# Performance work log

Measured on AMD Instinct MI355X. Metric: run time of the kernel, lower is better.

The kernel has to match this reference:

```python
import jax, jax.numpy as jnp
import numpy as np

B, P, E, D, A = 128, 196, 2048, 512, 512


def setup_inputs() -> dict:
    key = jax.random.key(0)
    ks = jax.random.split(key, 8)
    s = lambda fan_in: 1.0 / np.sqrt(fan_in)
    return {
        "encoder_out": jax.random.normal(ks[0], (B, P, E), jnp.float32),
        "decoder_hidden": jax.random.normal(ks[1], (B, D), jnp.float32),
        "We": jax.random.uniform(ks[2], (E, A), jnp.float32, -s(E), s(E)),
        "be": jax.random.uniform(ks[3], (A,), jnp.float32, -s(E), s(E)),
        "Wd": jax.random.uniform(ks[4], (D, A), jnp.float32, -s(D), s(D)),
        "bd": jax.random.uniform(ks[5], (A,), jnp.float32, -s(D), s(D)),
        "Wf": jax.random.uniform(ks[6], (A, 1), jnp.float32, -s(A), s(A)),
        "bf": jax.random.uniform(ks[7], (1,), jnp.float32, -s(A), s(A)),
    }


def reference(encoder_out, decoder_hidden, We, be, Wd, bd, Wf, bf):
    # att1: [B, P, A]
    att1 = jnp.einsum("bpe,ea->bpa", encoder_out, We) + be
    # att2: [B, A]
    att2 = decoder_hidden @ Wd + bd
    # additive attention scores: [B, P]
    att = (jax.nn.relu(att1 + att2[:, None, :]) @ Wf + bf)[..., 0]
    alpha = jax.nn.softmax(att, axis=1)  # softmax over pixels
    # weighted sum over pixels: [B, E]
    awe = jnp.einsum("bpe,bp->be", encoder_out, alpha)
    return awe, alpha
```

## Files before the change

### kernel.cpp

```cpp
#include <hip/hip_runtime.h>
#include <hip/hip_bf16.h>

typedef __attribute__((ext_vector_type(2))) unsigned int u32x2;
typedef __attribute__((ext_vector_type(4))) float f32x4;
typedef __attribute__((ext_vector_type(4))) unsigned int u32x4;
typedef __attribute__((ext_vector_type(8))) short s16x8;

#define B_  128
#define P_  196
#define E_  2048
#define D_  512
#define A_  512
#define M_  (B_*P_)
#define MT  112

typedef __attribute__((address_space(1))) const unsigned int gu32;
typedef __attribute__((address_space(3))) unsigned int lu32;
__device__ __forceinline__ void gl_lds16(const void* g, void* l) {
  __builtin_amdgcn_global_load_lds((gu32*)g, (lu32*)l, 16, 0, 0);
}

#define WAIT_VM3() asm volatile("s_waitcnt vmcnt(3)" ::: "memory")
#define WAIT_VM0() asm volatile("s_waitcnt vmcnt(0)" ::: "memory")
#define WAIT_LGKM0() asm volatile("s_waitcnt lgkmcnt(0)" ::: "memory")

__global__ void we_conv_kernel(const float* __restrict__ We,
                               unsigned short* __restrict__ WeTs) {
  __shared__ float tile[32][33];
  const int tx = threadIdx.x, ty = threadIdx.y;
  const int a0 = blockIdx.x * 32, e0 = blockIdx.y * 32;
  tile[ty][tx] = We[(e0 + ty) * A_ + a0 + tx];
  __syncthreads();
  const float v = tile[tx][ty];
  const unsigned int u = __float_as_uint(v);
  const unsigned short r = (unsigned short)((u + 0x7fffu + ((u >> 16) & 1u)) >> 16);
  const int a = a0 + ty;
  const int kt = blockIdx.y;
  const int c8 = tx >> 3, j = tx & 7;
  const int dest = ((a * 32 + c8 * 8) ^ ((a & 7) << 3)) + j;
  WeTs[kt * 16384 + dest] = r;
}

__global__ void att2_kernel(const float* __restrict__ h, const float* __restrict__ Wd,
                            const float* __restrict__ bd, const float* __restrict__ be,
                            float* __restrict__ att2pb) {
  const int b = blockIdx.x;
  const int t = threadIdx.x;
  __shared__ float hs[D_];
  hs[t] = h[b * D_ + t];
  hs[t + 256] = h[b * D_ + t + 256];
  __syncthreads();
  float a0 = 0.f, a1 = 0.f;
  for (int d = 0; d < D_; ++d) {
    const float hv = hs[d];
    a0 = fmaf(hv, Wd[d * A_ + t], a0);
    a1 = fmaf(hv, Wd[d * A_ + t + 256], a1);
  }
  att2pb[b * A_ + t] = a0 + bd[t] + be[t];
  att2pb[b * A_ + t + 256] = a1 + bd[t + 256] + be[t + 256];
}

__device__ inline unsigned pk2(float a, float b) {
  union { __hip_bfloat162 h; unsigned u; } cv;
  cv.h = __float22bfloat162_rn(make_float2(a, b));
  return cv.u;
}
__device__ __forceinline__ s16x8 ldsr(const unsigned short* p) {
  return *(const s16x8*)p;
}
#define MF(a, b, c) c = __builtin_amdgcn_mfma_f32_16x16x32_bf16(a, b, c, 0, 0, 0)

__launch_bounds__(1024, 4)
__global__ void score_kernel(const float* __restrict__ enc,
                             const unsigned short* __restrict__ WeTs,
                             const float* __restrict__ att2pb,
                             const float* __restrict__ Wf,
                             float* __restrict__ att_part) {
  __shared__ unsigned short Bh[3][512 * 32];
  __shared__ unsigned short Ahs[3][128 * 32];

  const int bid = blockIdx.x;
  const int m0 = bid * MT;

  const int t = threadIdx.x;
  const int lane = t & 63, w = t >> 6;
  const int wn = w * 32;

  const int ar = t >> 3, ac4 = t & 7;
  const int arc = ar < MT ? ar : MT - 1;
  const float* aptr = enc + (size_t)(m0 + arc) * E_ + ac4 * 4;
  const int awz = (ar * 32 + ac4 * 4) ^ ((ar & 7) << 3);

  const int doff = t * 8;

  const int q = lane >> 4, fr = lane & 15;
  const int fx = (fr & 7) << 3;
  int fa[7], fb[2];
#pragma unroll
  for (int i = 0; i < 7; ++i) fa[i] = ((i * 16 + fr) * 32 + q * 8) ^ fx;
#pragma unroll
  for (int j = 0; j < 2; ++j) fb[j] = ((wn + j * 16 + fr) * 32 + q * 8) ^ fx;

  const f32x4 zero = {0.f, 0.f, 0.f, 0.f};
  f32x4 acc[7][2];
#pragma unroll
  for (int mi = 0; mi < 7; ++mi) {
    acc[mi][0] = zero;
    acc[mi][1] = zero;
  }

  unsigned short *bAc = &Ahs[0][0], *bA1 = &Ahs[1][0], *bA2 = &Ahs[2][0];
  unsigned short *bBc = &Bh[0][0],  *bB1 = &Bh[1][0],  *bB2 = &Bh[2][0];

  f32x4 aC, aN;

  {
    aC = *(const f32x4*)(aptr);
    gl_lds16(WeTs + doff, bBc + doff);
    gl_lds16(WeTs + 8192 + doff, bBc + 8192 + doff);
    aN = *(const f32x4*)(aptr + 32);
    gl_lds16(WeTs + 16384 + doff, bB1 + doff);
    gl_lds16(WeTs + 16384 + 8192 + doff, bB1 + 8192 + doff);
    u32x2 av; av[0] = pk2(aC[0], aC[1]); av[1] = pk2(aC[2], aC[3]);
    *(u32x2*)(bAc + awz) = av;
    aC = aN;
    WAIT_VM3();
    WAIT_LGKM0();
    __builtin_amdgcn_s_barrier();
  }

  for (int it = 0; it < 62; ++it) {
    const int kof = (it + 2) * 32;
    aN = *(const f32x4*)(aptr + kof);
    const unsigned short* sb = WeTs + (size_t)(it + 2) * 16384;
    gl_lds16(sb + doff, bB2 + doff);
    gl_lds16(sb + 8192 + doff, bB2 + 8192 + doff);

    {
      s16x8 fbh0 = ldsr(bBc + fb[0]);
      s16x8 fbh1 = ldsr(bBc + fb[1]);
      __builtin_amdgcn_s_setprio(1);
#pragma unroll
      for (int mi = 0; mi < 7; ++mi) {
        const s16x8 fah = ldsr(bAc + fa[mi]);
        MF(fah, fbh0, acc[mi][0]);
        MF(fah, fbh1, acc[mi][1]);
      }
      __builtin_amdgcn_s_setprio(0);
    }

    {
      u32x2 av; av[0] = pk2(aC[0], aC[1]); av[1] = pk2(aC[2], aC[3]);
      *(u32x2*)(bA1 + awz) = av;
    }
    aC = aN;

    WAIT_VM3();
    WAIT_LGKM0();
    __builtin_amdgcn_s_barrier();

    unsigned short* tmp;
    tmp = bAc; bAc = bA1; bA1 = bA2; bA2 = tmp;
    tmp = bBc; bBc = bB1; bB1 = bB2; bB2 = tmp;
  }

  {
    s16x8 fbh0 = ldsr(bBc + fb[0]);
    s16x8 fbh1 = ldsr(bBc + fb[1]);
#pragma unroll
    for (int mi = 0; mi < 7; ++mi) {
      const s16x8 fah = ldsr(bAc + fa[mi]);
      MF(fah, fbh0, acc[mi][0]);
      MF(fah, fbh1, acc[mi][1]);
    }
    u32x2 av; av[0] = pk2(aC[0], aC[1]); av[1] = pk2(aC[2], aC[3]);
    *(u32x2*)(bA1 + awz) = av;
    WAIT_VM0();
    WAIT_LGKM0();
    __builtin_amdgcn_s_barrier();
  }

  {
    s16x8 fbh0 = ldsr(bB1 + fb[0]);
    s16x8 fbh1 = ldsr(bB1 + fb[1]);
#pragma unroll
    for (int mi = 0; mi < 7; ++mi) {
      const s16x8 fah = ldsr(bA1 + fa[mi]);
      MF(fah, fbh0, acc[mi][0]);
      MF(fah, fbh1, acc[mi][1]);
    }
  }

  const int colL = wn + fr;
  const float wf0 = Wf[colL], wf1 = Wf[colL + 16];
#pragma unroll
  for (int mi = 0; mi < 7; ++mi) {
    const int rowb = m0 + mi * 16 + (q << 2);
#pragma unroll
    for (int r = 0; r < 4; ++r) {
      const int row = rowb + r;
      const int bb = row / P_;
      const float* a2 = att2pb + bb * A_ + colL;
      float s = fmaxf(acc[mi][0][r] + a2[0], 0.f) * wf0
              + fmaxf(acc[mi][1][r] + a2[16], 0.f) * wf1;
#pragma unroll
      for (int off = 1; off < 16; off <<= 1) s += __shfl_xor(s, off);
      if (fr == 0) att_part[row * 16 + w] = s;
    }
  }
}

__global__ void softmax_awe_kernel(const float* __restrict__ enc,
                                   const float* __restrict__ att_part,
                                   float* __restrict__ out) {
  const int bid = blockIdx.x;
  const int b = bid >> 1, ch = bid & 1;
  const int t = threadIdx.x;
  __shared__ float sm[256];
  __shared__ float alpha_s[P_];

  float av = -1e30f;
  if (t < P_) {
    const float* apt = att_part + (b * P_ + t) * 16;
    float s = 0.f;
#pragma unroll
    for (int i = 0; i < 16; ++i) s += apt[i];
    av = s;
  }
  sm[t] = av;
  __syncthreads();
  for (int st = 128; st > 0; st >>= 1) {
    if (t < st) sm[t] = fmaxf(sm[t], sm[t + st]);
    __syncthreads();
  }
  const float mx = sm[0];
  __syncthreads();
  float ev = 0.f;
  if (t < P_) ev = __expf(av - mx);
  sm[t] = ev;
  __syncthreads();
  for (int st = 128; st > 0; st >>= 1) {
    if (t < st) sm[t] += sm[t + st];
    __syncthreads();
  }
  const float denom = sm[0];
  const float al = ev / denom;
  if (t < P_) {
    alpha_s[t] = al;
    if (ch == 0) out[B_ * E_ + b * P_ + t] = al;
  }
  __syncthreads();

  const int e0 = ch * 1024 + t * 4;
  const float* ebase = enc + (size_t)b * P_ * E_ + e0;
  f32x4 acc = {0.f, 0.f, 0.f, 0.f};
  for (int p = 0; p < P_; ++p) {
    const f32x4 v = *(const f32x4*)(ebase + (size_t)p * E_);
    const float a = alpha_s[p];
    acc.x += a * v.x; acc.y += a * v.y; acc.z += a * v.z; acc.w += a * v.w;
  }
  *(f32x4*)(out + b * E_ + e0) = acc;
}

extern "C" void kernel_launch(void* const* d_in, const int* in_sizes, int n_in,
                              void* d_out, int out_size, void* d_ws, size_t ws_size,
                              hipStream_t stream) {
  const float* enc = (const float*)d_in[0];
  const float* h   = (const float*)d_in[1];
  const float* We  = (const float*)d_in[2];
  const float* be  = (const float*)d_in[3];
  const float* Wd  = (const float*)d_in[4];
  const float* bd  = (const float*)d_in[5];
  const float* Wf  = (const float*)d_in[6];
  float* out = (float*)d_out;

  float* att2pb = (float*)d_ws;
  float* att_part = att2pb + B_ * A_;
  unsigned short* WeTs = (unsigned short*)(att_part + M_ * 16);

  we_conv_kernel<<<dim3(A_ / 32, E_ / 32), dim3(32, 32), 0, stream>>>(We, WeTs);
  att2_kernel<<<B_, 256, 0, stream>>>(h, Wd, bd, be, att2pb);
  score_kernel<<<M_ / MT, 1024, 0, stream>>>(enc, WeTs, att2pb, Wf, att_part);
  softmax_awe_kernel<<<B_ * 2, 256, 0, stream>>>(enc, att_part, out);
}
```

Before: 130.2 us.

## Load We fragments directly into registers instead of staging through LDS

```diff
diff --git a/kernel.cpp b/kernel.cpp
--- a/kernel.cpp
+++ b/kernel.cpp
@@ -3,7 +3,6 @@
 
 typedef __attribute__((ext_vector_type(2))) unsigned int u32x2;
 typedef __attribute__((ext_vector_type(4))) float f32x4;
-typedef __attribute__((ext_vector_type(4))) unsigned int u32x4;
 typedef __attribute__((ext_vector_type(8))) short s16x8;
 
 #define B_  128
@@ -14,18 +13,10 @@
 #define M_  (B_*P_)
 #define MT  112
 
-typedef __attribute__((address_space(1))) const unsigned int gu32;
-typedef __attribute__((address_space(3))) unsigned int lu32;
-__device__ __forceinline__ void gl_lds16(const void* g, void* l) {
-  __builtin_amdgcn_global_load_lds((gu32*)g, (lu32*)l, 16, 0, 0);
-}
-
-#define WAIT_VM3() asm volatile("s_waitcnt vmcnt(3)" ::: "memory")
-#define WAIT_VM0() asm volatile("s_waitcnt vmcnt(0)" ::: "memory")
 #define WAIT_LGKM0() asm volatile("s_waitcnt lgkmcnt(0)" ::: "memory")
 
 __global__ void we_conv_kernel(const float* __restrict__ We,
-                               unsigned short* __restrict__ WeTs) {
+                               unsigned short* __restrict__ WeTf) {
   __shared__ float tile[32][33];
   const int tx = threadIdx.x, ty = threadIdx.y;
   const int a0 = blockIdx.x * 32, e0 = blockIdx.y * 32;
@@ -36,9 +27,9 @@
   const unsigned short r = (unsigned short)((u + 0x7fffu + ((u >> 16) & 1u)) >> 16);
   const int a = a0 + ty;
   const int kt = blockIdx.y;
-  const int c8 = tx >> 3, j = tx & 7;
-  const int dest = ((a * 32 + c8 * 8) ^ ((a & 7) << 3)) + j;
-  WeTs[kt * 16384 + dest] = r;
+  const int q = tx >> 3, j = tx & 7;
+  const int nf = a >> 4, fr = a & 15;
+  WeTf[kt * 16384 + nf * 512 + (q * 16 + fr) * 8 + j] = r;
 }
 
 __global__ void att2_kernel(const float* __restrict__ h, const float* __restrict__ Wd,
@@ -72,11 +63,10 @@
 
 __launch_bounds__(1024, 4)
 __global__ void score_kernel(const float* __restrict__ enc,
-                             const unsigned short* __restrict__ WeTs,
+                             const unsigned short* __restrict__ WeTf,
                              const float* __restrict__ att2pb,
                              const float* __restrict__ Wf,
                              float* __restrict__ att_part) {
-  __shared__ unsigned short Bh[3][512 * 32];
   __shared__ unsigned short Ahs[3][128 * 32];
 
   const int bid = blockIdx.x;
@@ -91,15 +81,13 @@
   const float* aptr = enc + (size_t)(m0 + arc) * E_ + ac4 * 4;
   const int awz = (ar * 32 + ac4 * 4) ^ ((ar & 7) << 3);
 
-  const int doff = t * 8;
+  const unsigned short* bfp = WeTf + (w * 2) * 512 + lane * 8;
 
   const int q = lane >> 4, fr = lane & 15;
   const int fx = (fr & 7) << 3;
-  int fa[7], fb[2];
+  int fa[7];
 #pragma unroll
   for (int i = 0; i < 7; ++i) fa[i] = ((i * 16 + fr) * 32 + q * 8) ^ fx;
-#pragma unroll
-  for (int j = 0; j < 2; ++j) fb[j] = ((wn + j * 16 + fr) * 32 + q * 8) ^ fx;
 
   const f32x4 zero = {0.f, 0.f, 0.f, 0.f};
   f32x4 acc[7][2];
@@ -110,84 +98,71 @@
   }
 
   unsigned short *bAc = &Ahs[0][0], *bA1 = &Ahs[1][0], *bA2 = &Ahs[2][0];
-  unsigned short *bBc = &Bh[0][0],  *bB1 = &Bh[1][0],  *bB2 = &Bh[2][0];
-
   f32x4 aC, aN;
+  s16x8 bE0, bE1, bO0, bO1;
 
   {
     aC = *(const f32x4*)(aptr);
-    gl_lds16(WeTs + doff, bBc + doff);
-    gl_lds16(WeTs + 8192 + doff, bBc + 8192 + doff);
+    bE0 = ldsr(bfp);
+    bE1 = ldsr(bfp + 512);
     aN = *(const f32x4*)(aptr + 32);
-    gl_lds16(WeTs + 16384 + doff, bB1 + doff);
-    gl_lds16(WeTs + 16384 + 8192 + doff, bB1 + 8192 + doff);
+    bO0 = ldsr(bfp + 16384);
+    bO1 = ldsr(bfp + 16384 + 512);
     u32x2 av; av[0] = pk2(aC[0], aC[1]); av[1] = pk2(aC[2], aC[3]);
     *(u32x2*)(bAc + awz) = av;
     aC = aN;
-    WAIT_VM3();
     WAIT_LGKM0();
     __builtin_amdgcn_s_barrier();
   }
 
-  for (int it = 0; it < 62; ++it) {
-    const int kof = (it + 2) * 32;
-    aN = *(const f32x4*)(aptr + kof);
-    const unsigned short* sb = WeTs + (size_t)(it + 2) * 16384;
-    gl_lds16(sb + doff, bB2 + doff);
-    gl_lds16(sb + 8192 + doff, bB2 + 8192 + doff);
-
-    {
-      s16x8 fbh0 = ldsr(bBc + fb[0]);
-      s16x8 fbh1 = ldsr(bBc + fb[1]);
-      __builtin_amdgcn_s_setprio(1);
-#pragma unroll
-      for (int mi = 0; mi < 7; ++mi) {
-        const s16x8 fah = ldsr(bAc + fa[mi]);
-        MF(fah, fbh0, acc[mi][0]);
-        MF(fah, fbh1, acc[mi][1]);
-      }
-      __builtin_amdgcn_s_setprio(0);
+#define SUBITER(TT, BB0, BB1) {                                               \
+    aN = *(const f32x4*)(aptr + ((TT) + 2) * 32);                             \
+    __builtin_amdgcn_s_setprio(1);                                            \
+    _Pragma("unroll")                                                         \
+    for (int mi = 0; mi < 7; ++mi) {                                          \
+      const s16x8 fah = ldsr(bAc + fa[mi]);                                   \
+      MF(fah, BB0, acc[mi][0]);                                               \
+      MF(fah, BB1, acc[mi][1]);                                               \
+    }                                                                         \
+    __builtin_amdgcn_s_setprio(0);                                            \
+    BB0 = ldsr(bfp + ((TT) + 2) * 16384);                                     \
+    BB1 = ldsr(bfp + ((TT) + 2) * 16384 + 512);                               \
+    u32x2 av; av[0] = pk2(aC[0], aC[1]); av[1] = pk2(aC[2], aC[3]);           \
+    *(u32x2*)(bA1 + awz) = av;                                                \
+    aC = aN;                                                                  \
+    WAIT_LGKM0();                                                             \
+    __builtin_amdgcn_s_barrier();                                             \
+    unsigned short* tmp_ = bAc; bAc = bA1; bA1 = bA2; bA2 = tmp_;             \
+  }
+
+  for (int it = 0; it < 62; it += 2) {
+    SUBITER(it, bE0, bE1)
+    SUBITER(it + 1, bO0, bO1)
+  }
+#undef SUBITER
+
+  {
+    __builtin_amdgcn_s_setprio(1);
+#pragma unroll
+    for (int mi = 0; mi < 7; ++mi) {
+      const s16x8 fah = ldsr(bAc + fa[mi]);
+      MF(fah, bE0, acc[mi][0]);
+      MF(fah, bE1, acc[mi][1]);
     }
-
-    {
-      u32x2 av; av[0] = pk2(aC[0], aC[1]); av[1] = pk2(aC[2], aC[3]);
-      *(u32x2*)(bA1 + awz) = av;
-    }
-    aC = aN;
-
-    WAIT_VM3();
+    __builtin_amdgcn_s_setprio(0);
+    u32x2 av; av[0] = pk2(aC[0], aC[1]); av[1] = pk2(aC[2], aC[3]);
+    *(u32x2*)(bA1 + awz) = av;
     WAIT_LGKM0();
     __builtin_amdgcn_s_barrier();
-
-    unsigned short* tmp;
-    tmp = bAc; bAc = bA1; bA1 = bA2; bA2 = tmp;
-    tmp = bBc; bBc = bB1; bB1 = bB2; bB2 = tmp;
+    unsigned short* tmp_ = bAc; bAc = bA1; bA1 = bA2; bA2 = tmp_;
   }
 
   {
-    s16x8 fbh0 = ldsr(bBc + fb[0]);
-    s16x8 fbh1 = ldsr(bBc + fb[1]);
 #pragma unroll
     for (int mi = 0; mi < 7; ++mi) {
       const s16x8 fah = ldsr(bAc + fa[mi]);
-      MF(fah, fbh0, acc[mi][0]);
-      MF(fah, fbh1, acc[mi][1]);
-    }
-    u32x2 av; av[0] = pk2(aC[0], aC[1]); av[1] = pk2(aC[2], aC[3]);
-    *(u32x2*)(bA1 + awz) = av;
-    WAIT_VM0();
-    WAIT_LGKM0();
-    __builtin_amdgcn_s_barrier();
-  }
-
-  {
-    s16x8 fbh0 = ldsr(bB1 + fb[0]);
-    s16x8 fbh1 = ldsr(bB1 + fb[1]);
-#pragma unroll
-    for (int mi = 0; mi < 7; ++mi) {
-      const s16x8 fah = ldsr(bA1 + fa[mi]);
-      MF(fah, fbh0, acc[mi][0]);
-      MF(fah, fbh1, acc[mi][1]);
+      MF(fah, bO0, acc[mi][0]);
+      MF(fah, bO1, acc[mi][1]);
     }
   }
 
@@ -276,10 +251,10 @@
 
   float* att2pb = (float*)d_ws;
   float* att_part = att2pb + B_ * A_;
-  unsigned short* WeTs = (unsigned short*)(att_part + M_ * 16);
-
-  we_conv_kernel<<<dim3(A_ / 32, E_ / 32), dim3(32, 32), 0, stream>>>(We, WeTs);
+  unsigned short* WeTf = (unsigned short*)(att_part + M_ * 16);
+
+  we_conv_kernel<<<dim3(A_ / 32, E_ / 32), dim3(32, 32), 0, stream>>>(We, WeTf);
   att2_kernel<<<B_, 256, 0, stream>>>(h, Wd, bd, be, att2pb);
-  score_kernel<<<M_ / MT, 1024, 0, stream>>>(enc, WeTs, att2pb, Wf, att_part);
+  score_kernel<<<M_ / MT, 1024, 0, stream>>>(enc, WeTf, att2pb, Wf, att_part);
   softmax_awe_kernel<<<B_ * 2, 256, 0, stream>>>(enc, att_part, out);
 }
```

After: 119.0 us. 1.09x faster.
